# Performance work log

Measured on AMD Instinct MI355X. Metric: run time of the kernel, lower is better.

The kernel has to match this reference:

```python
import jax, jax.numpy as jnp
import numpy as np

N, E, IN, HID, OUT, H, R = 50000, 800000, 128, 64, 64, 4, 64
NEG_SLOPE = 0.2


def setup_inputs() -> dict:
    key = jax.random.key(0)
    ks = jax.random.split(key, 20)
    s = 0.05
    inp = {
        "x": jax.random.normal(ks[0], (N, IN), jnp.float32),
        "edge_index": jax.random.randint(ks[1], (2, E), 0, N, jnp.int32),
        "edge_type": jax.random.randint(ks[2], (E,), 0, R, jnp.int32),
        # layer 1 (in -> hidden)
        "rel1": jax.random.normal(ks[3], (R, IN), jnp.float32) * s,
        "W1": jax.random.normal(ks[4], (IN, H * HID), jnp.float32) * s,
        "We1": jax.random.normal(ks[5], (IN, H * HID), jnp.float32) * s,
        "as1": jax.random.normal(ks[6], (H, HID), jnp.float32) * s,
        "ad1": jax.random.normal(ks[7], (H, HID), jnp.float32) * s,
        "ae1": jax.random.normal(ks[8], (H, HID), jnp.float32) * s,
        "b1": jnp.zeros((HID,), jnp.float32),
        # layer 2 (hidden -> out)
        "rel2": jax.random.normal(ks[9], (R, HID), jnp.float32) * s,
        "W2": jax.random.normal(ks[10], (HID, H * OUT), jnp.float32) * s,
        "We2": jax.random.normal(ks[11], (HID, H * OUT), jnp.float32) * s,
        "as2": jax.random.normal(ks[12], (H, OUT), jnp.float32) * s,
        "ad2": jax.random.normal(ks[13], (H, OUT), jnp.float32) * s,
        "ae2": jax.random.normal(ks[14], (H, OUT), jnp.float32) * s,
        "b2": jnp.zeros((OUT,), jnp.float32),
    }
    return inp


def gat_layer(x, src, dst, edge_type, rel, W, We, a_s, a_d, a_e, b, C):
    # x: [N, Din] -> per-head features [N, H, C]
    xs = (x @ W).reshape(-1, H, C)
    alpha_src = jnp.einsum('nhc,hc->nh', xs, a_s)   # [N,H]
    alpha_dst = jnp.einsum('nhc,hc->nh', xs, a_d)   # [N,H]
    e = (rel[edge_type] @ We).reshape(-1, H, C)     # [E,H,C] projected edge feats
    alpha_e = jnp.einsum('ehc,hc->eh', e, a_e)      # [E,H]
    logits = alpha_src[src] + alpha_dst[dst] + alpha_e
    logits = jnp.where(logits >= 0, logits, NEG_SLOPE * logits)  # leaky_relu
    # segment softmax over destination nodes
    lmax = jax.ops.segment_max(logits, dst, num_segments=N)      # [N,H]
    ex = jnp.exp(logits - lmax[dst])
    den = jax.ops.segment_sum(ex, dst, num_segments=N)           # [N,H]
    w = ex / den[dst]                                            # [E,H]
    msg = w[:, :, None] * xs[src]                                # [E,H,C]
    out = jax.ops.segment_sum(msg, dst, num_segments=N)          # [N,H,C]
    return out.mean(axis=1) + b                                  # concat=False -> head mean


def reference(x, edge_index, edge_type, rel1, W1, We1, as1, ad1, ae1, b1,
              rel2, W2, We2, as2, ad2, ae2, b2):
    src, dst = edge_index[0], edge_index[1]
    h = gat_layer(x, src, dst, edge_type, rel1, W1, We1, as1, ad1, ae1, b1, HID)
    h = jax.nn.relu(h)
    out = gat_layer(h, src, dst, edge_type, rel2, W2, We2, as2, ad2, ae2, b2, OUT)
    return out
```

## Files before the change

### kernel.cpp

```cpp
#include <hip/hip_runtime.h>
#include <hip/hip_bf16.h>
#include <hip/hip_fp16.h>
#include <math.h>

#define N_NODES 50000
#define N_EDGES 800000
#define IN_DIM 128
#define NHEAD 4
#define NREL 64
#define HC 256
#define NEG_SLOPE 0.2f
#define SCAN_B ((N_NODES + 255) / 256)
#define XB (N_NODES / 16)
#define HB ((N_EDGES + 255) / 256)

using short8 = __attribute__((ext_vector_type(8))) short;
using f32x4  = __attribute__((ext_vector_type(4))) float;

__device__ __forceinline__ void load_lds16s(const short* g, short* l) {
  __builtin_amdgcn_global_load_lds(
      (const __attribute__((address_space(1))) unsigned int*)g,
      (__attribute__((address_space(3))) unsigned int*)l, 16, 0, 0);
}

__device__ __forceinline__ unsigned bf16rne(float v) {
  unsigned u = __float_as_uint(v);
  return (u + 0x7FFFu + ((u >> 16) & 1u)) >> 16;
}

__global__ __launch_bounds__(256) void hist_rank_kernel(
    const int* __restrict__ dst, int* __restrict__ deg,
    unsigned short* __restrict__ rank) {
  int e = blockIdx.x * blockDim.x + threadIdx.x;
  if (e < N_EDGES) {
    int r = atomicAdd(&deg[dst[e]], 1);
    rank[e] = (unsigned short)r;
  }
}

__global__ __launch_bounds__(256) void fused_prep(
    const float* __restrict__ x, short* __restrict__ xfh, short* __restrict__ xfl,
    const float* __restrict__ rel1, const float* __restrict__ We1, const float* __restrict__ ae1,
    const float* __restrict__ rel2, const float* __restrict__ We2, const float* __restrict__ ae2,
    float* __restrict__ tab1, float* __restrict__ tab2,
    const float* __restrict__ W1, short* __restrict__ w1h, short* __restrict__ w1l,
    const float* __restrict__ W2, short* __restrict__ w2h, short* __restrict__ w2l) {
  const int bid = blockIdx.x;
  const int t = threadIdx.x;
  __shared__ float plds[16 * 132];

  if (bid < XB) {
    const int K = IN_DIM, LW = K + 4;
    for (int i = t * 4; i < 16 * K; i += 1024) {
      int r = i / K, k = i - r * K;
      *(float4*)&plds[r * LW + k] = *(const float4*)&x[(size_t)(bid * 16 + r) * K + k];
    }
    __syncthreads();
    for (int c = t; c < 2 * K; c += 256) {
      int p_k = c >> 6, l = c & 63;
      int r = l & 15, k0 = p_k * 32 + (l >> 4) * 8;
      unsigned hp[4], lp[4];
#pragma unroll
      for (int q = 0; q < 4; ++q) {
        float v0 = plds[r * LW + k0 + q * 2];
        float v1 = plds[r * LW + k0 + q * 2 + 1];
        unsigned h0 = bf16rne(v0), h1 = bf16rne(v1);
        float l0 = (v0 - __uint_as_float(h0 << 16)) * 256.0f;
        float l1 = (v1 - __uint_as_float(h1 << 16)) * 256.0f;
        hp[q] = h0 | (h1 << 16);
        lp[q] = bf16rne(l0) | (bf16rne(l1) << 16);
      }
      size_t base = ((size_t)(bid * (K >> 5) + p_k) * 64 + l) * 8;
      *(int4*)&xfh[base] = make_int4(hp[0], hp[1], hp[2], hp[3]);
      *(int4*)&xfl[base] = make_int4(lp[0], lp[1], lp[2], lp[3]);
    }
    return;
  }
  if (bid < XB + 128) {
    const int rb = bid - XB;
    const int layer = rb >> 6, r = rb & 63;
    const float* rel = layer ? rel2 : rel1;
    const float* We  = layer ? We2  : We1;
    const float* ae  = layer ? ae2  : ae1;
    float* tab       = layer ? tab2 : tab1;
    const int K      = layer ? 64   : IN_DIM;
    float acc = 0.f;
    for (int k = 0; k < K; ++k) acc += rel[(size_t)r * K + k] * We[(size_t)k * HC + t];
    int h = t >> 6, lane = t & 63;
    float p = acc * ae[t];
#pragma unroll
    for (int off = 32; off > 0; off >>= 1) p += __shfl_down(p, off);
    if (lane == 0) tab[r * NHEAD + h] = p;
    return;
  }
  {
    const int wb = bid - (XB + 128);
    const float* W; short* Wh; short* Wl; int K, c;
    if (wb < 16) { W = W1; Wh = w1h; Wl = w1l; K = IN_DIM; c = wb * 256 + t; }
    else         { W = W2; Wh = w2h; Wl = w2l; K = 64;     c = (wb - 16) * 256 + t; }
    const int KP = K >> 5;
    if (c >= 16 * KP * 64) return;
    const int p = c >> 6, l = c & 63;
    const int p_c = p / KP, p_k = p - p_c * KP;
    const int col = p_c * 16 + (l & 15), k0 = p_k * 32 + (l >> 4) * 8;
    unsigned hp[4], lp[4];
#pragma unroll
    for (int q = 0; q < 4; ++q) {
      float v0 = W[(size_t)(k0 + q * 2) * HC + col];
      float v1 = W[(size_t)(k0 + q * 2 + 1) * HC + col];
      unsigned h0 = bf16rne(v0), h1 = bf16rne(v1);
      float l0 = (v0 - __uint_as_float(h0 << 16)) * 256.0f;
      float l1 = (v1 - __uint_as_float(h1 << 16)) * 256.0f;
      hp[q] = h0 | (h1 << 16);
      lp[q] = bf16rne(l0) | (bf16rne(l1) << 16);
    }
    size_t base = (size_t)c * 8;
    *(int4*)&Wh[base] = make_int4(hp[0], hp[1], hp[2], hp[3]);
    *(int4*)&Wl[base] = make_int4(lp[0], lp[1], lp[2], lp[3]);
  }
}

__global__ __launch_bounds__(256, 4) void gemm_mfma(
    const short* __restrict__ Xh, const short* __restrict__ Xl,
    const short* __restrict__ Wh, const short* __restrict__ Wl,
    const float* __restrict__ a_s, const float* __restrict__ a_d,
    __half2* __restrict__ xs16, float* __restrict__ asrc, float* __restrict__ adst,
    int M, int K) {
  __shared__ short lds[2][24 * 512];
  const int t = threadIdx.x;
  const int wv = t >> 6, l = t & 63;
  const int KP = K >> 5;
  const int pr0 = blockIdx.x * 4;
  const int pc0 = blockIdx.y * 8;
  const int c0 = blockIdx.y * 128;

#define STAGE(BI, PK)                                                         \
  {                                                                           \
    _Pragma("unroll")                                                         \
    for (int j = 0; j < 6; ++j) {                                             \
      const int s = wv * 6 + j;                                               \
      const short* srcp;                                                      \
      if (s < 4)       srcp = Xh + (((size_t)(pr0 + s) * KP + (PK)) << 9);    \
      else if (s < 8)  srcp = Xl + (((size_t)(pr0 + s - 4) * KP + (PK)) << 9);\
      else if (s < 16) srcp = Wh + (((size_t)(pc0 + s - 8) * KP + (PK)) << 9);\
      else             srcp = Wl + (((size_t)(pc0 + s - 16) * KP + (PK)) << 9);\
      load_lds16s(srcp + l * 8, &lds[BI][s * 512]);                           \
    }                                                                         \
  }

  f32x4 acc0[8], acc1[8];
#pragma unroll
  for (int i = 0; i < 8; ++i)
#pragma unroll
    for (int c = 0; c < 4; ++c) { acc0[i][c] = 0.f; acc1[i][c] = 0.f; }

  STAGE(0, 0);
  for (int pk = 0; pk < KP; ++pk) {
    const int cur = pk & 1;
    if (pk + 1 < KP) {
      STAGE(cur ^ 1, pk + 1);
      asm volatile("s_waitcnt vmcnt(6)" ::: "memory");
    } else {
      asm volatile("s_waitcnt vmcnt(0)" ::: "memory");
    }
    __builtin_amdgcn_s_barrier();
    __builtin_amdgcn_sched_barrier(0);
    const short8 ah = *(const short8*)&lds[cur][(0 + wv) * 512 + l * 8];
    const short8 al = *(const short8*)&lds[cur][(4 + wv) * 512 + l * 8];
#pragma unroll
    for (int t8 = 0; t8 < 8; ++t8) {
      const short8 bh = *(const short8*)&lds[cur][(8 + t8) * 512 + l * 8];
      const short8 bl = *(const short8*)&lds[cur][(16 + t8) * 512 + l * 8];
      acc0[t8] = __builtin_amdgcn_mfma_f32_16x16x32_bf16(ah, bh, acc0[t8], 0, 0, 0);
      acc1[t8] = __builtin_amdgcn_mfma_f32_16x16x32_bf16(ah, bl, acc1[t8], 0, 0, 0);
      acc1[t8] = __builtin_amdgcn_mfma_f32_16x16x32_bf16(al, bh, acc1[t8], 0, 0, 0);
    }
    asm volatile("" ::: "memory");
    __builtin_amdgcn_s_barrier();
  }
#undef STAGE

  const int col_l = l & 15;
  const int row_l = (l >> 4) * 4;
  __half* xsh = (__half*)xs16;
  float asv[8], adv[8];
#pragma unroll
  for (int t8 = 0; t8 < 8; ++t8) {
    asv[t8] = a_s[c0 + t8 * 16 + col_l];
    adv[t8] = a_d[c0 + t8 * 16 + col_l];
  }
  float sp[2][4], dp[2][4];
#pragma unroll
  for (int hl = 0; hl < 2; ++hl)
#pragma unroll
    for (int r = 0; r < 4; ++r) { sp[hl][r] = 0.f; dp[hl][r] = 0.f; }

#pragma unroll
  for (int t8 = 0; t8 < 8; ++t8) {
    const int hl = t8 >> 2;
#pragma unroll
    for (int r = 0; r < 4; ++r) {
      const float v = acc0[t8][r] + acc1[t8][r] * (1.0f / 256.0f);
      const int row = (pr0 + wv) * 16 + row_l + r;
      if (row < M) {
        const int col = c0 + t8 * 16 + col_l;
        xsh[(size_t)row * HC + col] = __float2half(v);
      }
      sp[hl][r] += v * asv[t8];
      dp[hl][r] += v * adv[t8];
    }
  }
#pragma unroll
  for (int off = 1; off < 16; off <<= 1) {
#pragma unroll
    for (int hl = 0; hl < 2; ++hl)
#pragma unroll
      for (int r = 0; r < 4; ++r) {
        sp[hl][r] += __shfl_xor(sp[hl][r], off);
        dp[hl][r] += __shfl_xor(dp[hl][r], off);
      }
  }
  if (col_l == 0) {
#pragma unroll
    for (int hl = 0; hl < 2; ++hl) {
      const int head = blockIdx.y * 2 + hl;
#pragma unroll
      for (int r = 0; r < 4; ++r) {
        const int row = (pr0 + wv) * 16 + row_l + r;
        if (row < M) {
          asrc[row * NHEAD + head] = sp[hl][r];
          adst[row * NHEAD + head] = dp[hl][r];
        }
      }
    }
  }
}

__global__ __launch_bounds__(256) void block_sum_kernel(
    const int* __restrict__ deg, int* __restrict__ bsum) {
  int i = blockIdx.x * 256 + threadIdx.x;
  int v = (i < N_NODES) ? deg[i] : 0;
#pragma unroll
  for (int off = 32; off > 0; off >>= 1) v += __shfl_down(v, off);
  __shared__ int w[4];
  if ((threadIdx.x & 63) == 0) w[threadIdx.x >> 6] = v;
  __syncthreads();
  if (threadIdx.x == 0) bsum[blockIdx.x] = w[0] + w[1] + w[2] + w[3];
}

__global__ __launch_bounds__(256) void scan_bsum_kernel(
    const int* __restrict__ bsum, int* __restrict__ boff) {
  __shared__ int s[256];
  int t = threadIdx.x;
  int v = (t < SCAN_B) ? bsum[t] : 0;
  s[t] = v;
  __syncthreads();
  for (int off = 1; off < 256; off <<= 1) {
    int u = (t >= off) ? s[t - off] : 0;
    __syncthreads();
    s[t] += u;
    __syncthreads();
  }
  boff[t] = (t == 0) ? 0 : s[t - 1];
}

__global__ __launch_bounds__(256) void scan_final_kernel(
    const int* __restrict__ deg, const int* __restrict__ boff,
    int* __restrict__ rowptr) {
  __shared__ int s[256];
  int t = threadIdx.x;
  int i = blockIdx.x * 256 + t;
  int v = (i < N_NODES) ? deg[i] : 0;
  s[t] = v;
  __syncthreads();
  for (int off = 1; off < 256; off <<= 1) {
    int u = (t >= off) ? s[t - off] : 0;
    __syncthreads();
    s[t] += u;
    __syncthreads();
  }
  int excl = boff[blockIdx.x] + s[t] - v;
  if (i < N_NODES) rowptr[i] = excl;
  if (t == 0 && blockIdx.x == 0) rowptr[N_NODES] = N_EDGES;
}

__global__ __launch_bounds__(256) void fill_kernel(
    const int* __restrict__ src, const int* __restrict__ dst,
    const int* __restrict__ etype, const unsigned short* __restrict__ rank,
    const int* __restrict__ rowptr, int* __restrict__ csrp) {
  int e = blockIdx.x * blockDim.x + threadIdx.x;
  if (e >= N_EDGES) return;
  int d = dst[e];
  int pos = rowptr[d] + rank[e];
  csrp[pos] = src[e] | (etype[e] << 16);
}

__global__ __launch_bounds__(256) void gat_node_kernel(
    const int* __restrict__ rowptr, const int* __restrict__ csr,
    const float* __restrict__ asrc, const float* __restrict__ adst,
    const float* __restrict__ tab, const __half2* __restrict__ xs16,
    const float* __restrict__ b, float* __restrict__ out,
    short* __restrict__ oxh, short* __restrict__ oxl, int mode) {
  const int n = (blockIdx.x * blockDim.x + threadIdx.x) >> 6;
  if (n >= N_NODES) return;
  const int lane = threadIdx.x & 63;
  const int hh = lane >> 4;
  const int cbase = lane << 2;
  const int i0 = rowptr[n], i1 = rowptr[n + 1];
  const float adn = adst[n * NHEAD + hh];
  const float treg = tab[lane * NHEAD + hh];

  float4 acc = make_float4(0.f, 0.f, 0.f, 0.f);
  float den = 0.f;
  int i = i0;
  for (; i + 4 <= i1; i += 4) {
    const int p0 = csr[i], p1 = csr[i + 1], p2 = csr[i + 2], p3 = csr[i + 3];
    const int s0 = p0 & 0xFFFF, s1 = p1 & 0xFFFF, s2 = p2 & 0xFFFF, s3 = p3 & 0xFFFF;
    float l0 = asrc[s0 * NHEAD + hh] + adn + __shfl(treg, p0 >> 16);
    float l1 = asrc[s1 * NHEAD + hh] + adn + __shfl(treg, p1 >> 16);
    float l2 = asrc[s2 * NHEAD + hh] + adn + __shfl(treg, p2 >> 16);
    float l3 = asrc[s3 * NHEAD + hh] + adn + __shfl(treg, p3 >> 16);
    const uint2 q0 = *(const uint2*)&xs16[((size_t)s0 * HC + cbase) >> 1];
    const uint2 q1 = *(const uint2*)&xs16[((size_t)s1 * HC + cbase) >> 1];
    const uint2 q2 = *(const uint2*)&xs16[((size_t)s2 * HC + cbase) >> 1];
    const uint2 q3 = *(const uint2*)&xs16[((size_t)s3 * HC + cbase) >> 1];
    l0 = (l0 >= 0.f) ? l0 : NEG_SLOPE * l0;
    l1 = (l1 >= 0.f) ? l1 : NEG_SLOPE * l1;
    l2 = (l2 >= 0.f) ? l2 : NEG_SLOPE * l2;
    l3 = (l3 >= 0.f) ? l3 : NEG_SLOPE * l3;
    const float w0 = __expf(l0), w1 = __expf(l1), w2 = __expf(l2), w3 = __expf(l3);
    den += (w0 + w1) + (w2 + w3);
    const float2 a0 = __half22float2(*(const __half2*)&q0.x), b0 = __half22float2(*(const __half2*)&q0.y);
    const float2 a1 = __half22float2(*(const __half2*)&q1.x), b1 = __half22float2(*(const __half2*)&q1.y);
    const float2 a2 = __half22float2(*(const __half2*)&q2.x), b2 = __half22float2(*(const __half2*)&q2.y);
    const float2 a3 = __half22float2(*(const __half2*)&q3.x), b3 = __half22float2(*(const __half2*)&q3.y);
    acc.x += w0 * a0.x + w1 * a1.x + w2 * a2.x + w3 * a3.x;
    acc.y += w0 * a0.y + w1 * a1.y + w2 * a2.y + w3 * a3.y;
    acc.z += w0 * b0.x + w1 * b1.x + w2 * b2.x + w3 * b3.x;
    acc.w += w0 * b0.y + w1 * b1.y + w2 * b2.y + w3 * b3.y;
  }
  for (; i < i1; ++i) {
    const int p = csr[i];
    const int s = p & 0xFFFF;
    float l = asrc[s * NHEAD + hh] + adn + __shfl(treg, p >> 16);
    l = (l >= 0.f) ? l : NEG_SLOPE * l;
    const float w = __expf(l);
    const uint2 q = *(const uint2*)&xs16[((size_t)s * HC + cbase) >> 1];
    const float2 a = __half22float2(*(const __half2*)&q.x);
    const float2 c = __half22float2(*(const __half2*)&q.y);
    den += w;
    acc.x += w * a.x; acc.y += w * a.y; acc.z += w * c.x; acc.w += w * c.y;
  }

  const float rd = (den > 0.f) ? (0.25f / den) : 0.f;
  float4 y = make_float4(acc.x * rd, acc.y * rd, acc.z * rd, acc.w * rd);
#pragma unroll
  for (int off = 16; off < 64; off <<= 1) {
    y.x += __shfl_xor(y.x, off);
    y.y += __shfl_xor(y.y, off);
    y.z += __shfl_xor(y.z, off);
    y.w += __shfl_xor(y.w, off);
  }
  if (lane < 16) {
    const float4 bb = *(const float4*)&b[lane * 4];
    y.x += bb.x; y.y += bb.y; y.z += bb.z; y.w += bb.w;
    if (mode) {
      y.x = fmaxf(y.x, 0.f); y.y = fmaxf(y.y, 0.f);
      y.z = fmaxf(y.z, 0.f); y.w = fmaxf(y.w, 0.f);
      unsigned h0 = bf16rne(y.x), h1 = bf16rne(y.y);
      unsigned h2 = bf16rne(y.z), h3 = bf16rne(y.w);
      float l0 = (y.x - __uint_as_float(h0 << 16)) * 256.0f;
      float l1 = (y.y - __uint_as_float(h1 << 16)) * 256.0f;
      float l2 = (y.z - __uint_as_float(h2 << 16)) * 256.0f;
      float l3 = (y.w - __uint_as_float(h3 << 16)) * 256.0f;
      unsigned hp0 = h0 | (h1 << 16), hp1 = h2 | (h3 << 16);
      unsigned lp0 = bf16rne(l0) | (bf16rne(l1) << 16);
      unsigned lp1 = bf16rne(l2) | (bf16rne(l3) << 16);
      const int pk = lane >> 3;
      const int lip = (n & 15) + ((lane >> 1) & 3) * 16;
      const int j0 = (lane & 1) * 4;
      size_t base = ((size_t)((n >> 4) * 2 + pk) * 64 + lip) * 8 + j0;
      *(uint2*)&oxh[base] = make_uint2(hp0, hp1);
      *(uint2*)&oxl[base] = make_uint2(lp0, lp1);
    } else {
      *(float4*)&out[(size_t)n * 64 + lane * 4] = y;
    }
  }
}

extern "C" void kernel_launch(void* const* d_in, const int* in_sizes, int n_in,
                              void* d_out, int out_size, void* d_ws, size_t ws_size,
                              hipStream_t stream) {
  const float* x   = (const float*)d_in[0];
  const int* eidx  = (const int*)d_in[1];
  const int* etype = (const int*)d_in[2];
  const float* rel1 = (const float*)d_in[3];
  const float* W1   = (const float*)d_in[4];
  const float* We1  = (const float*)d_in[5];
  const float* as1  = (const float*)d_in[6];
  const float* ad1  = (const float*)d_in[7];
  const float* ae1  = (const float*)d_in[8];
  const float* b1   = (const float*)d_in[9];
  const float* rel2 = (const float*)d_in[10];
  const float* W2   = (const float*)d_in[11];
  const float* We2  = (const float*)d_in[12];
  const float* as2  = (const float*)d_in[13];
  const float* ad2  = (const float*)d_in[14];
  const float* ae2  = (const float*)d_in[15];
  const float* b2   = (const float*)d_in[16];
  const int* src = eidx;
  const int* dst = eidx + N_EDGES;

  char* wsb = (char*)d_ws;
  size_t off = 0;
  auto carve = [&](size_t bytes) { char* p = wsb + off; off = (off + bytes + 255) & ~(size_t)255; return p; };
  __half2* xs16 = (__half2*)carve((size_t)N_NODES * HC * 2);
  float* asrc = (float*)carve((size_t)N_NODES * NHEAD * 4);
  float* adst = (float*)carve((size_t)N_NODES * NHEAD * 4);
  float* tab1 = (float*)carve(NREL * NHEAD * 4);
  float* tab2 = (float*)carve(NREL * NHEAD * 4);
  short* xfh  = (short*)carve(((size_t)N_NODES * IN_DIM + 32768) * 2);
  short* xfl  = (short*)carve(((size_t)N_NODES * IN_DIM + 32768) * 2);
  short* w1h  = (short*)carve(256 * IN_DIM * 2);
  short* w1l  = (short*)carve(256 * IN_DIM * 2);
  short* w2h  = (short*)carve(256 * 64 * 2);
  short* w2l  = (short*)carve(256 * 64 * 2);
  int* deg    = (int*)carve(N_NODES * 4);
  int* rowptr = (int*)carve((N_NODES + 1) * 4);
  unsigned short* rank = (unsigned short*)carve((size_t)N_EDGES * 2);
  int* csrp   = (int*)carve((size_t)N_EDGES * 4);
  int* bsum   = (int*)carve(256 * 4);
  int* boff   = (int*)carve(256 * 4);

  hipMemsetAsync(deg, 0, N_NODES * sizeof(int), stream);

  hist_rank_kernel<<<HB, 256, 0, stream>>>(dst, deg, rank);

  fused_prep<<<XB + 128 + 16 + 8, 256, 0, stream>>>(
      x, xfh, xfl,
      rel1, We1, ae1, rel2, We2, ae2, tab1, tab2,
      W1, w1h, w1l, W2, w2h, w2l);

  block_sum_kernel<<<SCAN_B, 256, 0, stream>>>(deg, bsum);
  scan_bsum_kernel<<<1, 256, 0, stream>>>(bsum, boff);
  scan_final_kernel<<<SCAN_B, 256, 0, stream>>>(deg, boff, rowptr);
  fill_kernel<<<HB, 256, 0, stream>>>(src, dst, etype, rank, rowptr, csrp);

  const dim3 gemm_grid((N_NODES + 63) / 64, 2);
  const int GB = (N_NODES * 64 + 255) / 256;

  gemm_mfma<<<gemm_grid, 256, 0, stream>>>(xfh, xfl, w1h, w1l, as1, ad1, xs16, asrc, adst, N_NODES, IN_DIM);
  gat_node_kernel<<<GB, 256, 0, stream>>>(rowptr, csrp, asrc, adst, tab1, xs16,
                                          b1, nullptr, xfh, xfl, 1);

  gemm_mfma<<<gemm_grid, 256, 0, stream>>>(xfh, xfl, w2h, w2l, as2, ad2, xs16, asrc, adst, N_NODES, 64);
  gat_node_kernel<<<GB, 256, 0, stream>>>(rowptr, csrp, asrc, adst, tab2, xs16,
                                          b2, (float*)d_out, nullptr, nullptr, 0);
}
```

Measured before the change: 273.2 us.

## Compute edge attention logits cooperatively per 16-edge chunk and fuse fp16 FMA

The node-aggregation kernel previously had each lane recompute the logit and exp for every edge of its own head. It now processes edges in 16-edge chunks, with each lane computing one (edge, head) logit and exp. Source ids and weights are then broadcast by shuffles, and the fp16 features are accumulated with v_fma_mix_f32 inline asm instead of separate convert and FMA. The relation table moves into LDS, and the denominator is reduced across lanes at the end. This removes redundant exp and asrc loads per lane, at the cost of a block-level sync, extra shuffles, and a serialized loop over partial chunks.

```diff
diff --git a/kernel.cpp b/kernel.cpp
--- a/kernel.cpp
+++ b/kernel.cpp
@@ -301,57 +301,58 @@
     const float* __restrict__ tab, const __half2* __restrict__ xs16,
     const float* __restrict__ b, float* __restrict__ out,
     short* __restrict__ oxh, short* __restrict__ oxl, int mode) {
-  const int n = (blockIdx.x * blockDim.x + threadIdx.x) >> 6;
+  __shared__ float lds_tab[NREL * NHEAD];
+  const int t = threadIdx.x;
+  lds_tab[t] = tab[t];
+  __syncthreads();
+  const int n = (blockIdx.x * blockDim.x + t) >> 6;
   if (n >= N_NODES) return;
-  const int lane = threadIdx.x & 63;
-  const int hh = lane >> 4;
-  const int cbase = lane << 2;
+  const int lane = t & 63;
+  const int hlog = lane & 3;
+  const int eoff = lane >> 2;
+  const int hpay = lane >> 4;
+  const unsigned voff = (unsigned)lane * 2;
   const int i0 = rowptr[n], i1 = rowptr[n + 1];
-  const float adn = adst[n * NHEAD + hh];
-  const float treg = tab[lane * NHEAD + hh];
+  const float adn = adst[n * NHEAD + hlog];
 
   float4 acc = make_float4(0.f, 0.f, 0.f, 0.f);
-  float den = 0.f;
-  int i = i0;
-  for (; i + 4 <= i1; i += 4) {
-    const int p0 = csr[i], p1 = csr[i + 1], p2 = csr[i + 2], p3 = csr[i + 3];
-    const int s0 = p0 & 0xFFFF, s1 = p1 & 0xFFFF, s2 = p2 & 0xFFFF, s3 = p3 & 0xFFFF;
-    float l0 = asrc[s0 * NHEAD + hh] + adn + __shfl(treg, p0 >> 16);
-    float l1 = asrc[s1 * NHEAD + hh] + adn + __shfl(treg, p1 >> 16);
-    float l2 = asrc[s2 * NHEAD + hh] + adn + __shfl(treg, p2 >> 16);
-    float l3 = asrc[s3 * NHEAD + hh] + adn + __shfl(treg, p3 >> 16);
-    const uint2 q0 = *(const uint2*)&xs16[((size_t)s0 * HC + cbase) >> 1];
-    const uint2 q1 = *(const uint2*)&xs16[((size_t)s1 * HC + cbase) >> 1];
-    const uint2 q2 = *(const uint2*)&xs16[((size_t)s2 * HC + cbase) >> 1];
-    const uint2 q3 = *(const uint2*)&xs16[((size_t)s3 * HC + cbase) >> 1];
-    l0 = (l0 >= 0.f) ? l0 : NEG_SLOPE * l0;
-    l1 = (l1 >= 0.f) ? l1 : NEG_SLOPE * l1;
-    l2 = (l2 >= 0.f) ? l2 : NEG_SLOPE * l2;
-    l3 = (l3 >= 0.f) ? l3 : NEG_SLOPE * l3;
-    const float w0 = __expf(l0), w1 = __expf(l1), w2 = __expf(l2), w3 = __expf(l3);
-    den += (w0 + w1) + (w2 + w3);
-    const float2 a0 = __half22float2(*(const __half2*)&q0.x), b0 = __half22float2(*(const __half2*)&q0.y);
-    const float2 a1 = __half22float2(*(const __half2*)&q1.x), b1 = __half22float2(*(const __half2*)&q1.y);
-    const float2 a2 = __half22float2(*(const __half2*)&q2.x), b2 = __half22float2(*(const __half2*)&q2.y);
-    const float2 a3 = __half22float2(*(const __half2*)&q3.x), b3 = __half22float2(*(const __half2*)&q3.y);
-    acc.x += w0 * a0.x + w1 * a1.x + w2 * a2.x + w3 * a3.x;
-    acc.y += w0 * a0.y + w1 * a1.y + w2 * a2.y + w3 * a3.y;
-    acc.z += w0 * b0.x + w1 * b1.x + w2 * b2.x + w3 * b3.x;
-    acc.w += w0 * b0.y + w1 * b1.y + w2 * b2.y + w3 * b3.y;
-  }
-  for (; i < i1; ++i) {
-    const int p = csr[i];
-    const int s = p & 0xFFFF;
-    float l = asrc[s * NHEAD + hh] + adn + __shfl(treg, p >> 16);
-    l = (l >= 0.f) ? l : NEG_SLOPE * l;
-    const float w = __expf(l);
-    const uint2 q = *(const uint2*)&xs16[((size_t)s * HC + cbase) >> 1];
-    const float2 a = __half22float2(*(const __half2*)&q.x);
-    const float2 c = __half22float2(*(const __half2*)&q.y);
-    den += w;
-    acc.x += w * a.x; acc.y += w * a.y; acc.z += w * c.x; acc.w += w * c.y;
-  }
-
+  float denp = 0.f;
+
+  for (int base = i0; base < i1; base += 16) {
+    const int nE = min(16, i1 - base);
+    float w = 0.f;
+    int sreg = 0;
+    if (eoff < nE) {
+      const int p = csr[base + eoff];
+      const int s = p & 0xFFFF;
+      sreg = s;
+      const int r = p >> 16;
+      float l = asrc[s * NHEAD + hlog] + adn + lds_tab[r * NHEAD + hlog];
+      l = fmaxf(l, NEG_SLOPE * l);
+      w = __expf(l);
+    }
+    denp += w;
+#pragma unroll
+    for (int k = 0; k < 16; ++k) {
+      if (k < nE) {
+        const int s_k = __shfl(sreg, k * 4);
+        const float w_k = __shfl(w, k * 4 + hpay);
+        const uint2 q = *(const uint2*)&xs16[((unsigned)s_k << 7) + voff];
+        asm volatile(
+            "v_fma_mix_f32 %0, %2, %3, %0 op_sel_hi:[0,1,0]\n\t"
+            "v_fma_mix_f32 %1, %2, %3, %1 op_sel:[0,1,0] op_sel_hi:[0,1,0]"
+            : "+v"(acc.x), "+v"(acc.y) : "v"(w_k), "v"(q.x));
+        asm volatile(
+            "v_fma_mix_f32 %0, %2, %3, %0 op_sel_hi:[0,1,0]\n\t"
+            "v_fma_mix_f32 %1, %2, %3, %1 op_sel:[0,1,0] op_sel_hi:[0,1,0]"
+            : "+v"(acc.z), "+v"(acc.w) : "v"(w_k), "v"(q.y));
+      }
+    }
+  }
+
+#pragma unroll
+  for (int off = 4; off < 64; off <<= 1) denp += __shfl_xor(denp, off);
+  const float den = __shfl(denp, hpay);
   const float rd = (den > 0.f) ? (0.25f / den) : 0.f;
   float4 y = make_float4(acc.x * rd, acc.y * rd, acc.z * rd, acc.w * rd);
 #pragma unroll
```

New measurement: 299.3 us. +9.6%, slower.
